# Optimization experiments

Measured on AMD Instinct MI355X. Metric: run time of the kernel, lower is better.

Reference implementation:

```python
import jax, jax.numpy as jnp
import numpy as np

N_ATOMS = 100_000  # number of center atoms
K = 16             # neighbors per atom within cutoff (uniform for static shapes)


def setup_inputs() -> dict:
    # pair_i: sorted center-atom index per neighbor pair, K neighbors per atom.
    pair_i = jnp.repeat(jnp.arange(N_ATOMS, dtype=jnp.int32), K)  # [N_ATOMS*K]
    return {"pair_i": pair_i, "n_atoms": N_ATOMS, "max_neighbors": K}


def reference(pair_i, n_atoms, max_neighbors):
    """Segmented combinations: for each atom's contiguous neighbor block,
    emit all unique (j,k) pair-index combinations, exactly matching the
    torch.combinations lexicographic order of the original Python loop.
    Assumes uniform neighbor count == max_neighbors (as built in setup)."""
    ones = jnp.ones_like(pair_i)
    counts = jax.ops.segment_sum(ones, pair_i, num_segments=n_atoms)  # [n_atoms]
    starts = jnp.cumsum(counts) - counts                              # block offsets (prefix sum)

    # within-block combination template, shared by all atoms
    pu, pv = jnp.triu_indices(max_neighbors, k=1)  # [T_per], T_per = K*(K-1)/2
    t_per = pu.shape[0]

    idx_i = jnp.repeat(jnp.arange(n_atoms, dtype=pair_i.dtype), t_per)          # [n_atoms*T_per]
    idx_j = (starts[:, None] + pu[None, :]).reshape(-1).astype(pair_i.dtype)    # [n_atoms*T_per]
    idx_k = (starts[:, None] + pv[None, :]).reshape(-1).astype(pair_i.dtype)    # [n_atoms*T_per]
    return idx_i, idx_j, idx_k
```

## Files before the change

### kernel.cpp

```cpp
#include <hip/hip_runtime.h>


constexpr int K      = 16;
constexpr int T_PER  = K * (K - 1) / 2;
constexpr int GROUPS = T_PER / 4;

typedef int iv4 __attribute__((ext_vector_type(4)));

struct Tbl { unsigned u[GROUPS]; unsigned v[GROUPS]; };
constexpr Tbl make_tbl() {
    Tbl t{};
    int idx = 0;
    for (int a = 0; a < K; ++a)
        for (int b = a + 1; b < K; ++b) {
            t.u[idx / 4] |= (unsigned)a << ((idx % 4) * 8);
            t.v[idx / 4] |= (unsigned)b << ((idx % 4) * 8);
            ++idx;
        }
    return t;
}
__device__ constexpr Tbl TBL = make_tbl();

__global__ void starts_kernel(const int* __restrict__ pair_i, int* __restrict__ starts,
                              int n_atoms, int m) {
    int a = blockIdx.x * blockDim.x + threadIdx.x;
    if (a >= n_atoms) return;
    int lo = 0, hi = m;
    while (lo < hi) {
        int mid = (lo + hi) >> 1;
        if (pair_i[mid] < a) lo = mid + 1; else hi = mid;
    }
    starts[a] = lo;
}

__global__ __launch_bounds__(256)
void gen_split(const int* __restrict__ starts, int* __restrict__ out,
               int per_arr_groups) {
    const int s      = blockIdx.x % 3;
    const int b      = blockIdx.x / 3;
    const int nb3    = gridDim.x / 3;
    const int stride = nb3 * blockDim.x;

    iv4* o = (iv4*)out + (size_t)s * per_arr_groups;

    if (s == 0) {
        for (int g = b * blockDim.x + threadIdx.x; g < per_arr_groups; g += stride) {
            const int atom = g / GROUPS;
            iv4 v; v[0] = atom; v[1] = atom; v[2] = atom; v[3] = atom;
            o[g] = v;
        }
    } else {
        const unsigned* __restrict__ tb = (s == 1) ? TBL.u : TBL.v;
        for (int g = b * blockDim.x + threadIdx.x; g < per_arr_groups; g += stride) {
            const int atom  = g / GROUPS;
            const int r     = g - atom * GROUPS;
            const int start = starts[atom];
            const unsigned ub = tb[r];
            iv4 v;
            v[0] = start + (int)(ub & 0xff);
            v[1] = start + (int)((ub >> 8)  & 0xff);
            v[2] = start + (int)((ub >> 16) & 0xff);
            v[3] = start + (int)((ub >> 24) & 0xff);
            o[g] = v;
        }
    }
}

extern "C" void kernel_launch(void* const* d_in, const int* in_sizes, int n_in,
                              void* d_out, int out_size, void* d_ws, size_t ws_size,
                              hipStream_t stream) {
    const int* pair_i  = (const int*)d_in[0];
    const int  m       = in_sizes[0];
    const int  n_atoms = m / K;

    int* out = (int*)d_out;
    const int per_arr_groups = n_atoms * GROUPS;

    int* starts = (int*)d_ws;
    {
        const int b1 = 256;
        starts_kernel<<<(n_atoms + b1 - 1) / b1, b1, 0, stream>>>(pair_i, starts, n_atoms, m);
    }

    gen_split<<<3072, 256, 0, stream>>>(starts, out, per_arr_groups);
}
```

Baseline: 155.9 us.

## Assign contiguous chunks per block and stage starts/table in LDS

Replaces the grid-stride loop with fixed contiguous chunks of 12 iterations per block, fully unrolled in the common case. Each block loads the starts for its range of atoms and the combination table into shared memory once, then reads them from LDS instead of global/constant memory. This is meant to cut redundant global loads and loop overhead and improve write locality, at the cost of a sync and a tail path.

```diff
diff --git a/kernel.cpp b/kernel.cpp
--- a/kernel.cpp
+++ b/kernel.cpp
@@ -4,6 +4,9 @@
 constexpr int K      = 16;
 constexpr int T_PER  = K * (K - 1) / 2;
 constexpr int GROUPS = T_PER / 4;
+constexpr int BLK    = 256;
+constexpr int ITERS  = 12;
+constexpr int CHUNK  = BLK * ITERS;
 
 typedef int iv4 __attribute__((ext_vector_type(4)));
 
@@ -33,29 +36,67 @@
     starts[a] = lo;
 }
 
-__global__ __launch_bounds__(256)
+__global__ __launch_bounds__(BLK)
 void gen_split(const int* __restrict__ starts, int* __restrict__ out,
                int per_arr_groups) {
-    const int s      = blockIdx.x % 3;
-    const int b      = blockIdx.x / 3;
-    const int nb3    = gridDim.x / 3;
-    const int stride = nb3 * blockDim.x;
+    const int s  = blockIdx.x % 3;
+    const int b  = blockIdx.x / 3;
+    const int g0 = b * CHUNK;
+    if (g0 >= per_arr_groups) return;
 
-    iv4* o = (iv4*)out + (size_t)s * per_arr_groups;
+    iv4* __restrict__ o = (iv4*)out + (size_t)s * per_arr_groups;
+    const bool full = (g0 + CHUNK) <= per_arr_groups;
 
     if (s == 0) {
-        for (int g = b * blockDim.x + threadIdx.x; g < per_arr_groups; g += stride) {
-            const int atom = g / GROUPS;
-            iv4 v; v[0] = atom; v[1] = atom; v[2] = atom; v[3] = atom;
+        if (full) {
+            #pragma unroll
+            for (int k = 0; k < ITERS; ++k) {
+                const int g    = g0 + k * BLK + (int)threadIdx.x;
+                const int atom = g / GROUPS;
+                iv4 v; v[0] = atom; v[1] = atom; v[2] = atom; v[3] = atom;
+                o[g] = v;
+            }
+        } else {
+            for (int g = g0 + (int)threadIdx.x; g < per_arr_groups; g += BLK) {
+                const int atom = g / GROUPS;
+                iv4 v; v[0] = atom; v[1] = atom; v[2] = atom; v[3] = atom;
+                o[g] = v;
+            }
+        }
+        return;
+    }
+
+    __shared__ int      s_st[CHUNK / GROUPS + 2];
+    __shared__ unsigned s_tb[GROUPS];
+    const int gend = full ? (g0 + CHUNK) : per_arr_groups;
+    const int a0   = g0 / GROUPS;
+    const int a1   = (gend - 1) / GROUPS;
+    const int na   = a1 - a0 + 1;
+    if ((int)threadIdx.x < na)     s_st[threadIdx.x] = starts[a0 + (int)threadIdx.x];
+    if ((int)threadIdx.x < GROUPS) s_tb[threadIdx.x] = (s == 1 ? TBL.u : TBL.v)[threadIdx.x];
+    __syncthreads();
+
+    if (full) {
+        #pragma unroll
+        for (int k = 0; k < ITERS; ++k) {
+            const int g     = g0 + k * BLK + (int)threadIdx.x;
+            const int atom  = g / GROUPS;
+            const int r     = g - atom * GROUPS;
+            const int start = s_st[atom - a0];
+            const unsigned ub = s_tb[r];
+            iv4 v;
+            v[0] = start + (int)(ub & 0xff);
+            v[1] = start + (int)((ub >> 8)  & 0xff);
+            v[2] = start + (int)((ub >> 16) & 0xff);
+            v[3] = start + (int)((ub >> 24) & 0xff);
             o[g] = v;
         }
     } else {
-        const unsigned* __restrict__ tb = (s == 1) ? TBL.u : TBL.v;
-        for (int g = b * blockDim.x + threadIdx.x; g < per_arr_groups; g += stride) {
+        for (int g = g0 + (int)threadIdx.x; g < gend; g += BLK) {
             const int atom  = g / GROUPS;
             const int r     = g - atom * GROUPS;
-            const int start = starts[atom];
-            const unsigned ub = tb[r];
+            const int start = s_st[atom - a0];
+            const unsigned ub = s_tb[r];
             iv4 v;
             v[0] = start + (int)(ub & 0xff);
             v[1] = start + (int)((ub >> 8)  & 0xff);
@@ -82,5 +123,6 @@
         starts_kernel<<<(n_atoms + b1 - 1) / b1, b1, 0, stream>>>(pair_i, starts, n_atoms, m);
     }
 
-    gen_split<<<3072, 256, 0, stream>>>(starts, out, per_arr_groups);
+    const int nbs  = (per_arr_groups + CHUNK - 1) / CHUNK;
+    gen_split<<<3 * nbs, BLK, 0, stream>>>(starts, out, per_arr_groups);
 }
```

Result: no change. 158.9 us (+1.9%).
